# Performance work log

Measured on AMD Instinct MI355X. Metric: run time of the kernel, lower is better.

Reference implementation:

```python
import jax, jax.numpy as jnp
import numpy as np

D_IN = 1024
D_OUT = 1024

def setup_inputs() -> dict:
    key = jax.random.key(0)
    kx, kq, kk, kv = jax.random.split(key, 4)
    scale = 1.0 / np.sqrt(D_IN)
    return {
        "x": jax.random.normal(kx, (4, 4096, D_IN), dtype=jnp.float32),
        "W_q": jax.random.uniform(kq, (D_IN, D_OUT), dtype=jnp.float32, minval=-scale, maxval=scale),
        "W_k": jax.random.uniform(kk, (D_IN, D_OUT), dtype=jnp.float32, minval=-scale, maxval=scale),
        "W_v": jax.random.uniform(kv, (D_IN, D_OUT), dtype=jnp.float32, minval=-scale, maxval=scale),
    }

def reference(x, W_q, W_k, W_v):
    # x: [b, s, d_in]; weights stored as [d_in, d_out] (transposed vs torch Linear)
    Q = jnp.einsum('bsd,de->bse', x, W_q)
    K = jnp.einsum('bsd,de->bse', x, W_k)
    V = jnp.einsum('bsd,de->bse', x, W_v)
    d_k = K.shape[-1]
    scores = jnp.einsum('bqe,bke->bqk', Q, K) / jnp.sqrt(jnp.asarray(d_k, x.dtype))
    weights = jax.nn.softmax(scores, axis=-1)
    return jnp.einsum('bqk,bke->bqe', weights, V)
```

## Files before the change

kernel.cpp:

```cpp
#include <hip/hip_runtime.h>

typedef unsigned short u16;
typedef float f32x4 __attribute__((ext_vector_type(4)));
typedef u16   u16x4 __attribute__((ext_vector_type(4)));
typedef u16   u16x8 __attribute__((ext_vector_type(8)));
typedef __bf16 bf16x8 __attribute__((ext_vector_type(8)));

static __device__ __forceinline__ u16 f2bf(float x) {
    unsigned int u = __builtin_bit_cast(unsigned int, x);
    u = (u + 0x7FFFu + ((u >> 16) & 1u)) >> 16;
    return (u16)u;
}
static __device__ __forceinline__ float bf2f(u16 x) {
    unsigned int u = ((unsigned int)x) << 16;
    return __builtin_bit_cast(float, u);
}
static __device__ __forceinline__ bf16x8 as_bf(u16x8 v) { return __builtin_bit_cast(bf16x8, v); }

static __device__ __forceinline__ void gload16(const u16* g, u16* lds) {
    __builtin_amdgcn_global_load_lds(
        (const __attribute__((address_space(1))) void*)g,
        (__attribute__((address_space(3))) void*)lds,
        16, 0, 0);
}

#define KSCALE 0.045084220027780106f

#define STAGE_G2L(dst, src, stride, ROUNDS) do {                               \
    _Pragma("unroll") for (int i_ = 0; i_ < (ROUNDS); ++i_) {                  \
        int c_ = (i_ * 4 + w) * 64 + l;                                        \
        int row_ = c_ >> 3, c8_ = c_ & 7;                                      \
        gload16((src) + (size_t)row_ * (stride) + ((c8_ ^ (row_ & 7)) << 3),   \
                &(dst)[(i_ * 4 + w) * 512]);                                   \
    } } while (0)

__global__ __launch_bounds__(256) void wt_kernel(const float* __restrict__ Wq,
                                                 const float* __restrict__ Wk,
                                                 const float* __restrict__ Wv,
                                                 u16* __restrict__ Wt) {
    __shared__ float tile[64][65];
    const int mat = blockIdx.z;
    const float* W = (mat == 0) ? Wq : ((mat == 1) ? Wk : Wv);
    const int bx = blockIdx.x, by = blockIdx.y;
    const int tid = threadIdx.x;
#pragma unroll
    for (int i = 0; i < 16; ++i) {
        int idx = i * 256 + tid;
        int r = idx >> 6, c = idx & 63;
        tile[r][c] = W[(by * 64 + r) * 1024 + bx * 64 + c];
    }
    __syncthreads();
#pragma unroll
    for (int i = 0; i < 16; ++i) {
        int idx = i * 256 + tid;
        int r = idx >> 6, c = idx & 63;
        Wt[mat * 1048576 + (bx * 64 + r) * 1024 + by * 64 + c] = f2bf(tile[c][r]);
    }
}

__global__ __launch_bounds__(256, 3) void qkv_gemm(const float* __restrict__ X,
                                                   const u16* __restrict__ Wt,
                                                   u16* __restrict__ Qo,
                                                   u16* __restrict__ Ko,
                                                   u16* __restrict__ Vt) {
    __shared__ u16 As[128 * 64];
    __shared__ u16 Bs[128 * 64];
    const int bid = blockIdx.x;
    const int swz = (bid & 7) * 96 + (bid >> 3);
    const int bm = swz / 24, bn = swz % 24;
    const int tid = threadIdx.x;
    const int w = tid >> 6, l = tid & 63, lg = l >> 4, lr = l & 15;
    const int wr = w >> 1, wc = w & 1;

    const f32x4 z4 = {0.f, 0.f, 0.f, 0.f};
    f32x4 acc[4][4];
#pragma unroll
    for (int m = 0; m < 4; ++m)
#pragma unroll
        for (int n = 0; n < 4; ++n) acc[m][n] = z4;

    for (int kb = 0; kb < 16; ++kb) {
        __syncthreads();
        STAGE_G2L(Bs, Wt + (size_t)(bn * 128) * 1024 + kb * 64, 1024, 4);
#pragma unroll
        for (int i = 0; i < 4; ++i) {
            int cid = i * 256 + tid;
            int row = cid >> 3, c8 = cid & 7;
            const float* src = X + (bm * 128 + row) * 1024 + kb * 64 + c8 * 8;
            f32x4 v0 = *(const f32x4*)(src);
            f32x4 v1 = *(const f32x4*)(src + 4);
            u16x8 t;
            t[0] = f2bf(v0[0]); t[1] = f2bf(v0[1]); t[2] = f2bf(v0[2]); t[3] = f2bf(v0[3]);
            t[4] = f2bf(v1[0]); t[5] = f2bf(v1[1]); t[6] = f2bf(v1[2]); t[7] = f2bf(v1[3]);
            *(u16x8*)(&As[row * 64 + ((c8 ^ (row & 7)) << 3)]) = t;
        }
        __syncthreads();
#pragma unroll
        for (int kk = 0; kk < 2; ++kk) {
            bf16x8 af[4], bfr[4];
#pragma unroll
            for (int m = 0; m < 4; ++m) {
                int row = wr * 64 + m * 16 + lr;
                af[m] = as_bf(*(const u16x8*)(&As[row * 64 + (((kk * 4 + lg) ^ (lr & 7)) << 3)]));
            }
#pragma unroll
            for (int n = 0; n < 4; ++n) {
                int row = wc * 64 + n * 16 + lr;
                bfr[n] = as_bf(*(const u16x8*)(&Bs[row * 64 + (((kk * 4 + lg) ^ (lr & 7)) << 3)]));
            }
#pragma unroll
            for (int m = 0; m < 4; ++m)
#pragma unroll
                for (int n = 0; n < 4; ++n)
                    acc[m][n] = __builtin_amdgcn_mfma_f32_16x16x32_bf16(af[m], bfr[n], acc[m][n], 0, 0, 0);
        }
    }
    const int row0 = bm * 128 + wr * 64;
    const int col0 = bn * 128 + wc * 64;
#pragma unroll
    for (int m = 0; m < 4; ++m) {
#pragma unroll
        for (int n = 0; n < 4; ++n) {
            int col = col0 + n * 16 + lr;
            int mat = col >> 10;
            int cg = col & 1023;
            int row = row0 + m * 16 + lg * 4;
            if (mat == 2) {
                u16x4 v;
                v[0] = f2bf(acc[m][n][0]); v[1] = f2bf(acc[m][n][1]);
                v[2] = f2bf(acc[m][n][2]); v[3] = f2bf(acc[m][n][3]);
                *(u16x4*)(Vt + cg * 4096 + row) = v;
            } else {
                u16* P = mat ? Ko : Qo;
#pragma unroll
                for (int r = 0; r < 4; ++r) P[(row + r) * 1024 + cg] = f2bf(acc[m][n][r]);
            }
        }
    }
}

__global__ __launch_bounds__(256, 4) void qk_gemm(const u16* __restrict__ Qb,
                                                  const u16* __restrict__ Kb,
                                                  u16* __restrict__ P) {
    __shared__ u16 As[128 * 64];
    __shared__ u16 Bs[128 * 64];
    const int bid = blockIdx.x;
    const int swz = (bid & 7) * 128 + (bid >> 3);
    const int bm = swz >> 5, bn = swz & 31;
    const int tid = threadIdx.x;
    const int w = tid >> 6, l = tid & 63, lg = l >> 4, lr = l & 15;
    const int wr = w >> 1, wc = w & 1;

    const f32x4 z4 = {0.f, 0.f, 0.f, 0.f};
    f32x4 acc[4][4];
#pragma unroll
    for (int m = 0; m < 4; ++m)
#pragma unroll
        for (int n = 0; n < 4; ++n) acc[m][n] = z4;

    for (int kb = 0; kb < 16; ++kb) {
        __syncthreads();
        STAGE_G2L(As, Qb + (size_t)(bm * 128) * 1024 + kb * 64, 1024, 4);
        STAGE_G2L(Bs, Kb + (size_t)(bn * 128) * 1024 + kb * 64, 1024, 4);
        __syncthreads();
#pragma unroll
        for (int kk = 0; kk < 2; ++kk) {
            bf16x8 af[4], bfr[4];
#pragma unroll
            for (int m = 0; m < 4; ++m) {
                int row = wr * 64 + m * 16 + lr;
                af[m] = as_bf(*(const u16x8*)(&As[row * 64 + (((kk * 4 + lg) ^ (lr & 7)) << 3)]));
            }
#pragma unroll
            for (int n = 0; n < 4; ++n) {
                int row = wc * 64 + n * 16 + lr;
                bfr[n] = as_bf(*(const u16x8*)(&Bs[row * 64 + (((kk * 4 + lg) ^ (lr & 7)) << 3)]));
            }
#pragma unroll
            for (int m = 0; m < 4; ++m)
#pragma unroll
                for (int n = 0; n < 4; ++n)
                    acc[m][n] = __builtin_amdgcn_mfma_f32_16x16x32_bf16(af[m], bfr[n], acc[m][n], 0, 0, 0);
        }
    }
    const int row0 = bm * 128 + wr * 64;
    const int col0 = bn * 128 + wc * 64;
#pragma unroll
    for (int m = 0; m < 4; ++m) {
#pragma unroll
        for (int r = 0; r < 4; ++r) {
            const size_t rowg = (size_t)(row0 + m * 16 + lg * 4 + r);
#pragma unroll
            for (int n = 0; n < 4; ++n)
                P[rowg * 4096 + col0 + n * 16 + lr] = f2bf(exp2f(acc[m][n][r] * KSCALE));
        }
    }
}

__global__ __launch_bounds__(256) void rowsum_pair(const u16* __restrict__ P0,
                                                   const u16* __restrict__ P1,
                                                   float* __restrict__ rlb) {
    const int gw = blockIdx.x * 4 + (threadIdx.x >> 6);
    const int l = threadIdx.x & 63;
    const u16* P = (gw < 4096) ? P0 : P1;
    const u16* pr = P + (size_t)(gw & 4095) * 4096 + l * 8;
    float s = 0.f;
#pragma unroll
    for (int j = 0; j < 8; ++j) {
        u16x8 v = *(const u16x8*)(pr + j * 512);
#pragma unroll
        for (int e = 0; e < 8; ++e) s += bf2f(v[e]);
    }
    s += __shfl_xor(s, 1, 64);
    s += __shfl_xor(s, 2, 64);
    s += __shfl_xor(s, 4, 64);
    s += __shfl_xor(s, 8, 64);
    s += __shfl_xor(s, 16, 64);
    s += __shfl_xor(s, 32, 64);
    if (l == 0) rlb[gw] = 1.0f / s;
}

__global__ __launch_bounds__(256, 4) void pv_pair(const u16* __restrict__ P0,
                                                  const u16* __restrict__ P1,
                                                  const u16* __restrict__ V0,
                                                  const u16* __restrict__ V1,
                                                  const float* __restrict__ rlb,
                                                  float* __restrict__ Out0,
                                                  float* __restrict__ Out1) {
    __shared__ u16 As[128 * 64];
    __shared__ u16 Bs[128 * 64];
    __shared__ float rl_s[128];
    const int bid = blockIdx.x;
    const int swz = (bid & 7) * 64 + (bid >> 3);
    const int bb = swz >> 8, rem = swz & 255;
    const int bm = rem >> 3, bn = rem & 7;
    const int q0 = bm * 128, e0 = bn * 128;
    const u16* P  = bb ? P1 : P0;
    const u16* Vt = bb ? V1 : V0;
    float* Out    = bb ? Out1 : Out0;
    const int tid = threadIdx.x;
    const int w = tid >> 6, l = tid & 63, lg = l >> 4, lr = l & 15;
    const int wr = w >> 1, wc = w & 1;

    if (tid < 128) rl_s[tid] = rlb[bb * 4096 + q0 + tid];

    const f32x4 z4 = {0.f, 0.f, 0.f, 0.f};
    f32x4 acc[4][4];
#pragma unroll
    for (int m = 0; m < 4; ++m)
#pragma unroll
        for (int n = 0; n < 4; ++n) acc[m][n] = z4;

    for (int kb = 0; kb < 64; ++kb) {
        __syncthreads();
        STAGE_G2L(As, P + (size_t)q0 * 4096 + kb * 64, 4096, 4);
        STAGE_G2L(Bs, Vt + (size_t)e0 * 4096 + kb * 64, 4096, 4);
        __syncthreads();
#pragma unroll
        for (int kk = 0; kk < 2; ++kk) {
            bf16x8 af[4], bfr[4];
#pragma unroll
            for (int m = 0; m < 4; ++m) {
                int row = wr * 64 + m * 16 + lr;
                af[m] = as_bf(*(const u16x8*)(&As[row * 64 + (((kk * 4 + lg) ^ (lr & 7)) << 3)]));
            }
#pragma unroll
            for (int n = 0; n < 4; ++n) {
                int row = wc * 64 + n * 16 + lr;
                bfr[n] = as_bf(*(const u16x8*)(&Bs[row * 64 + (((kk * 4 + lg) ^ (lr & 7)) << 3)]));
            }
#pragma unroll
            for (int m = 0; m < 4; ++m)
#pragma unroll
                for (int n = 0; n < 4; ++n)
                    acc[m][n] = __builtin_amdgcn_mfma_f32_16x16x32_bf16(af[m], bfr[n], acc[m][n], 0, 0, 0);
        }
    }
#pragma unroll
    for (int m = 0; m < 4; ++m) {
#pragma unroll
        for (int r = 0; r < 4; ++r) {
            int rloc = wr * 64 + m * 16 + lg * 4 + r;
            float rl = rl_s[rloc];
#pragma unroll
            for (int n = 0; n < 4; ++n)
                Out[(size_t)(q0 + rloc) * 1024 + e0 + wc * 64 + n * 16 + lr] = acc[m][n][r] * rl;
        }
    }
}

extern "C" void kernel_launch(void* const* d_in, const int* in_sizes, int n_in,
                              void* d_out, int out_size, void* d_ws, size_t ws_size,
                              hipStream_t stream) {
    const float* x  = (const float*)d_in[0];
    const float* Wq = (const float*)d_in[1];
    const float* Wk = (const float*)d_in[2];
    const float* Wv = (const float*)d_in[3];
    float* out = (float*)d_out;

    char* ws = (char*)d_ws;
    u16* Wt = (u16*)(ws);
    u16* Qb = (u16*)(ws + 6291456);
    u16* Kb = (u16*)(ws + 14680064);
    u16* V0 = (u16*)(ws + 23068672);
    u16* V1 = (u16*)(ws + 31457280);
    u16* P0 = (u16*)(ws + 39845888);
    u16* P1 = (u16*)(ws + 73400320);
    float* rlb = (float*)Qb;

    wt_kernel<<<dim3(16, 16, 3), 256, 0, stream>>>(Wq, Wk, Wv, Wt);
    for (int p = 0; p < 2; ++p) {
        const float* x0 = x + (size_t)(2 * p) * 4194304;
        const float* x1 = x + (size_t)(2 * p + 1) * 4194304;
        float* o0 = out + (size_t)(2 * p) * 4194304;
        float* o1 = out + (size_t)(2 * p + 1) * 4194304;
        qkv_gemm<<<dim3(768), 256, 0, stream>>>(x0, Wt, Qb, Kb, V0);
        qk_gemm<<<dim3(1024), 256, 0, stream>>>(Qb, Kb, P0);
        qkv_gemm<<<dim3(768), 256, 0, stream>>>(x1, Wt, Qb, Kb, V1);
        qk_gemm<<<dim3(1024), 256, 0, stream>>>(Qb, Kb, P1);
        rowsum_pair<<<dim3(2048), 256, 0, stream>>>(P0, P1, rlb);
        pv_pair<<<dim3(512), 256, 0, stream>>>(P0, P1, V0, V1, rlb, o0, o1);
    }
}
```

Baseline: 458.6 us.

## Replace QK^T GEMM with 256x256-tile, 4-stage pipelined 512-thread kernel

Rewrites the Q·K^T score kernel to use 256x256 output tiles with 8 waves and a 4-deep LDS ring buffer. Global-to-LDS loads are issued three k-steps ahead and gated by explicit vmcnt waits with a single barrier per step. MFMA issue priority is raised to keep the compute pipe fed. The aim is to cut global traffic per FLOP and hide load latency. In exchange it uses more registers (32 accumulators per wave), more LDS, and fewer blocks (256), which may hurt occupancy or tail balance.

After: 489.7 us. 6.8% more time.

```diff
diff --git a/kernel.cpp b/kernel.cpp
--- a/kernel.cpp
+++ b/kernel.cpp
@@ -139,60 +139,80 @@
     }
 }
 
-__global__ __launch_bounds__(256, 4) void qk_gemm(const u16* __restrict__ Qb,
-                                                  const u16* __restrict__ Kb,
-                                                  u16* __restrict__ P) {
-    __shared__ u16 As[128 * 64];
-    __shared__ u16 Bs[128 * 64];
+__global__ __launch_bounds__(512, 2) void qk_8ph(const u16* __restrict__ Qb,
+                                                 const u16* __restrict__ Kb,
+                                                 u16* __restrict__ P) {
+    __shared__ u16 lds[4][32 * 512];
     const int bid = blockIdx.x;
-    const int swz = (bid & 7) * 128 + (bid >> 3);
-    const int bm = swz >> 5, bn = swz & 31;
+    const int swz = (bid & 7) * 32 + (bid >> 3);
+    const int bm = swz >> 4, bn = swz & 15;
     const int tid = threadIdx.x;
     const int w = tid >> 6, l = tid & 63, lg = l >> 4, lr = l & 15;
-    const int wr = w >> 1, wc = w & 1;
+    const int wr = w >> 2, wc = w & 3;
+
+    const u16* gsrc[4];
+#pragma unroll
+    for (int i = 0; i < 4; ++i) {
+        int f = w * 4 + i;
+        const u16* base = (f < 16) ? (Qb + (size_t)(bm * 256 + f * 16) * 1024)
+                                   : (Kb + (size_t)(bn * 256 + (f - 16) * 16) * 1024);
+        gsrc[i] = base + (size_t)lr * 1024 + lg * 8;
+    }
+
+#define STAGE8(kt) do {                                                        \
+    u16* dst_ = &lds[(kt) & 3][w * 4 * 512];                                   \
+    _Pragma("unroll") for (int i_ = 0; i_ < 4; ++i_)                           \
+        gload16(gsrc[i_] + (kt) * 32, dst_ + i_ * 512);                        \
+    } while (0)
 
     const f32x4 z4 = {0.f, 0.f, 0.f, 0.f};
-    f32x4 acc[4][4];
-#pragma unroll
-    for (int m = 0; m < 4; ++m)
-#pragma unroll
-        for (int n = 0; n < 4; ++n) acc[m][n] = z4;
-
-    for (int kb = 0; kb < 16; ++kb) {
-        __syncthreads();
-        STAGE_G2L(As, Qb + (size_t)(bm * 128) * 1024 + kb * 64, 1024, 4);
-        STAGE_G2L(Bs, Kb + (size_t)(bn * 128) * 1024 + kb * 64, 1024, 4);
-        __syncthreads();
-#pragma unroll
-        for (int kk = 0; kk < 2; ++kk) {
-            bf16x8 af[4], bfr[4];
-#pragma unroll
-            for (int m = 0; m < 4; ++m) {
-                int row = wr * 64 + m * 16 + lr;
-                af[m] = as_bf(*(const u16x8*)(&As[row * 64 + (((kk * 4 + lg) ^ (lr & 7)) << 3)]));
-            }
-#pragma unroll
-            for (int n = 0; n < 4; ++n) {
-                int row = wc * 64 + n * 16 + lr;
-                bfr[n] = as_bf(*(const u16x8*)(&Bs[row * 64 + (((kk * 4 + lg) ^ (lr & 7)) << 3)]));
-            }
-#pragma unroll
-            for (int m = 0; m < 4; ++m)
-#pragma unroll
-                for (int n = 0; n < 4; ++n)
-                    acc[m][n] = __builtin_amdgcn_mfma_f32_16x16x32_bf16(af[m], bfr[n], acc[m][n], 0, 0, 0);
-        }
-    }
-    const int row0 = bm * 128 + wr * 64;
-    const int col0 = bn * 128 + wc * 64;
-#pragma unroll
-    for (int m = 0; m < 4; ++m) {
+    f32x4 acc[8][4];
+#pragma unroll
+    for (int mi = 0; mi < 8; ++mi)
+#pragma unroll
+        for (int ni = 0; ni < 4; ++ni) acc[mi][ni] = z4;
+
+    STAGE8(0); STAGE8(1); STAGE8(2);
+
+#pragma unroll
+    for (int kt = 0; kt < 32; ++kt) {
+        if (kt <= 29)      asm volatile("s_waitcnt vmcnt(8)" ::: "memory");
+        else if (kt == 30) asm volatile("s_waitcnt vmcnt(4)" ::: "memory");
+        else               asm volatile("s_waitcnt vmcnt(0)" ::: "memory");
+        __builtin_amdgcn_sched_barrier(0);
+        __builtin_amdgcn_s_barrier();
+        __builtin_amdgcn_sched_barrier(0);
+        if (kt < 29) STAGE8(kt + 3);
+        const u16* A = &lds[kt & 3][0];
+        const u16* B = &lds[kt & 3][16 * 512];
+        bf16x8 bfr[4];
+#pragma unroll
+        for (int ni = 0; ni < 4; ++ni)
+            bfr[ni] = as_bf(*(const u16x8*)(B + (wc * 4 + ni) * 512 + l * 8));
+        bf16x8 af[8];
+#pragma unroll
+        for (int mi = 0; mi < 8; ++mi)
+            af[mi] = as_bf(*(const u16x8*)(A + (wr * 8 + mi) * 512 + l * 8));
+        __builtin_amdgcn_s_setprio(1);
+#pragma unroll
+        for (int mi = 0; mi < 8; ++mi)
+#pragma unroll
+            for (int ni = 0; ni < 4; ++ni)
+                acc[mi][ni] = __builtin_amdgcn_mfma_f32_16x16x32_bf16(af[mi], bfr[ni], acc[mi][ni], 0, 0, 0);
+        __builtin_amdgcn_s_setprio(0);
+    }
+#undef STAGE8
+
+    const int row0 = bm * 256 + wr * 128;
+    const int col0 = bn * 256 + wc * 64;
+#pragma unroll
+    for (int mi = 0; mi < 8; ++mi) {
 #pragma unroll
         for (int r = 0; r < 4; ++r) {
-            const size_t rowg = (size_t)(row0 + m * 16 + lg * 4 + r);
-#pragma unroll
-            for (int n = 0; n < 4; ++n)
-                P[rowg * 4096 + col0 + n * 16 + lr] = f2bf(exp2f(acc[m][n][r] * KSCALE));
+            const size_t rowg = (size_t)(row0 + mi * 16 + lg * 4 + r);
+#pragma unroll
+            for (int ni = 0; ni < 4; ++ni)
+                P[rowg * 4096 + col0 + ni * 16 + lr] = f2bf(exp2f(acc[mi][ni][r] * KSCALE));
         }
     }
 }
@@ -315,9 +335,9 @@
         float* o0 = out + (size_t)(2 * p) * 4194304;
         float* o1 = out + (size_t)(2 * p + 1) * 4194304;
         qkv_gemm<<<dim3(768), 256, 0, stream>>>(x0, Wt, Qb, Kb, V0);
-        qk_gemm<<<dim3(1024), 256, 0, stream>>>(Qb, Kb, P0);
+        qk_8ph<<<dim3(256), 512, 0, stream>>>(Qb, Kb, P0);
         qkv_gemm<<<dim3(768), 256, 0, stream>>>(x1, Wt, Qb, Kb, V1);
-        qk_gemm<<<dim3(1024), 256, 0, stream>>>(Qb, Kb, P1);
+        qk_8ph<<<dim3(256), 512, 0, stream>>>(Qb, Kb, P1);
         rowsum_pair<<<dim3(2048), 256, 0, stream>>>(P0, P1, rlb);
         pv_pair<<<dim3(512), 256, 0, stream>>>(P0, P1, V0, V1, rlb, o0, o1);
     }
```
